# Performance work log

Measured on AMD Instinct MI355X. Metric: run time of the kernel, lower is better.

Reference implementation:

```python
import jax, jax.numpy as jnp
import numpy as np

DIM = 64
HID = 2 * DIM  # ffn_expansion_factor hard-coded to 2 in __init__


def _conv(x, w, b, pad, groups=1):
    # x: [N,C,H,W], w: [O, C//groups, kh, kw] (torch OIHW layout)
    y = jax.lax.conv_general_dilated(
        x, w, window_strides=(1, 1), padding=[(pad, pad), (pad, pad)],
        feature_group_count=groups,
        dimension_numbers=('NCHW', 'OIHW', 'NCHW'))
    return y + b[None, :, None, None]


def setup_inputs() -> dict:
    key = jax.random.key(0)
    ks = jax.random.split(key, 16)
    s = 0.05
    B, H, W = 4, 256, 256
    return {
        'x': jax.random.normal(ks[0], (B, DIM, H, W), jnp.float32),
        'pneffectiveness': jax.random.normal(ks[1], (B, 2, H, W), jnp.float32),
        # project_in: dim -> 2*hidden, 1x1
        'w_in': jax.random.normal(ks[2], (2 * HID, DIM, 1, 1), jnp.float32) * s,
        'b_in': jax.random.normal(ks[3], (2 * HID,), jnp.float32) * s,
        # project_in_pn: 2 -> hidden, 1x1
        'w_pn': jax.random.normal(ks[4], (HID, 2, 1, 1), jnp.float32) * s,
        'b_pn': jax.random.normal(ks[5], (HID,), jnp.float32) * s,
        # dwconvI: 3*hidden -> hidden, 3x3, groups=hidden (3 in-ch per group)
        'w_dw1': jax.random.normal(ks[6], (HID, 3, 3, 3), jnp.float32) * s,
        'b_dw1': jax.random.normal(ks[7], (HID,), jnp.float32) * s,
        # dwconvIII[0]: 3*hidden -> hidden, 3x3, groups=hidden
        'w_dw3a': jax.random.normal(ks[8], (HID, 3, 3, 3), jnp.float32) * s,
        'b_dw3a': jax.random.normal(ks[9], (HID,), jnp.float32) * s,
        # dwconvIII[1]: hidden -> hidden depthwise 3x3
        'w_dw3b': jax.random.normal(ks[10], (HID, 1, 3, 3), jnp.float32) * s,
        'b_dw3b': jax.random.normal(ks[11], (HID,), jnp.float32) * s,
        # project_out: hidden -> dim, 1x1, groups=2
        'w_out': jax.random.normal(ks[12], (DIM, HID // 2, 1, 1), jnp.float32) * s,
        'b_out': jax.random.normal(ks[13], (DIM,), jnp.float32) * s,
    }


def reference(x, pneffectiveness, w_in, b_in, w_pn, b_pn, w_dw1, b_dw1,
              w_dw3a, b_dw3a, w_dw3b, b_dw3b, w_out, b_out):
    xi = _conv(x, w_in, b_in, pad=0)                    # [B, 2*HID, H, W]
    pn = _conv(pneffectiveness, w_pn, b_pn, pad=0)      # [B, HID, H, W]
    xc = jnp.concatenate([pn, xi], axis=1)              # [B, 3*HID, H, W]
    d1 = _conv(xc, w_dw1, b_dw1, pad=1, groups=HID)     # [B, HID, H, W]
    d3 = _conv(xc, w_dw3a, b_dw3a, pad=1, groups=HID)
    d3 = _conv(d3, w_dw3b, b_dw3b, pad=1, groups=HID)   # [B, HID, H, W]
    x1_a, x1_b = jnp.split(d1, 2, axis=1)
    x2_a, x2_b = jnp.split(d3, 2, axis=1)
    x1 = jnp.concatenate([x1_a, x2_a], axis=1)          # [B, HID, H, W]
    x2 = jnp.concatenate([x1_b, x2_b], axis=1)
    g = jax.nn.gelu(x1, approximate=False) * x2         # exact GELU like F.gelu
    return _conv(g, w_out, b_out, pad=0, groups=2)      # [B, DIM, H, W]
```

## Files before the change

kernel.cpp:

```cpp
#include <hip/hip_runtime.h>
#include <hip/hip_bf16.h>


#define T 16
#define R20 20
#define R18 18
#define HW 65536
#define XC_BYTES ((size_t)4 * 16 * HW * 24 * 2)

typedef unsigned short u16;
typedef unsigned int u32;

typedef __attribute__((ext_vector_type(8))) short bf16x8;
typedef __attribute__((ext_vector_type(4))) float f32x4;
typedef __attribute__((ext_vector_type(2))) float f32x2;

__device__ __forceinline__ float bflo(u32 w) {
    union { u32 i; float f; } v; v.i = w << 16; return v.f;
}
__device__ __forceinline__ float bfhi(u32 w) {
    union { u32 i; float f; } v; v.i = w & 0xffff0000u; return v.f;
}
__device__ __forceinline__ float bf2f(u16 u) {
    union { u32 i; float f; } v; v.i = ((u32)u) << 16; return v.f;
}
__device__ __forceinline__ u16 f2bf(float f) {
    union { float f; u32 i; } v; v.f = f;
    u32 x = v.i;
    u32 r = (x + 0x7fffu + ((x >> 16) & 1u)) >> 16;
    return (u16)r;
}
__device__ __forceinline__ u32 f2bf2(float a, float b) {
    return (u32)f2bf(a) | ((u32)f2bf(b) << 16);
}
__device__ __forceinline__ float gelu_exact(float v) {
    return 0.5f * v * (1.0f + erff(v * 0.70710678118654752f));
}
__device__ __forceinline__ float erf_fast(float x) {
    float ax = fabsf(x);
    float t = __builtin_amdgcn_rcpf(fmaf(0.3275911f, ax, 1.0f));
    float p = fmaf(t, 1.061405429f, -1.453152027f);
    p = fmaf(t, p, 1.421413741f);
    p = fmaf(t, p, -0.284496736f);
    p = fmaf(t, p, 0.254829592f);
    p = p * t;
    float e = __expf(-ax * ax);
    float r = fmaf(-p, e, 1.0f);
    return copysignf(r, x);
}
__device__ __forceinline__ float gelu_fast(float v) {
    return 0.5f * v * (1.0f + erf_fast(v * 0.70710678118654752f));
}

__device__ __forceinline__ void pack_pair(float a, float b, u32& hi, u32& lo) {
    union { float f; u32 i; } ua, ub, ha, hb, la, lb;
    ua.f = a; ub.f = b;
    ha.i = ua.i & 0xffff0000u;
    hb.i = ub.i & 0xffff0000u;
    hi = (ha.i >> 16) | hb.i;
    la.f = a - ha.f;
    lb.f = b - hb.f;
    lo = (la.i >> 16) | (lb.i & 0xffff0000u);
}

__global__ __launch_bounds__(256, 2)
void k1_proj_mfma(const float* __restrict__ xin,
                  const float* __restrict__ pnin,
                  const float* __restrict__ w_in,
                  const float* __restrict__ b_in,
                  const float* __restrict__ w_pn,
                  const float* __restrict__ b_pn,
                  u16* __restrict__ xc)
{
    __shared__ float s_x[64][65];
    __shared__ float s_bin[256];

    const int tid  = threadIdx.x;
    const int b    = blockIdx.y;
    const int px0  = blockIdx.x * 64;
    const int lane = tid & 63;
    const int wid  = tid >> 6;
    const int lr   = lane & 15;
    const int lh   = lane >> 4;
    const int CB   = wid * 64;

    s_bin[tid] = b_in[tid];

    {
        const float* xb = xin + (size_t)b * 64 * HW + px0;
#pragma unroll
        for (int i = 0; i < 4; ++i) {
            int idx = tid + 256 * i;
            int row = idx >> 4, seg = (idx & 15) * 4;
            float4 v = *(const float4*)(xb + (size_t)row * HW + seg);
            s_x[row][seg + 0] = v.x; s_x[row][seg + 1] = v.y;
            s_x[row][seg + 2] = v.z; s_x[row][seg + 3] = v.w;
        }
    }

    bf16x8 whi[4][2], wlo[4][2];
#pragma unroll
    for (int ci = 0; ci < 4; ++ci)
#pragma unroll
        for (int ks = 0; ks < 2; ++ks) {
            const float* wp = w_in + (size_t)(CB + 16 * ci + lr) * 64
                            + 32 * ks + 8 * lh;
            float4 A0 = *(const float4*)wp;
            float4 A1 = *(const float4*)(wp + 4);
            union { u32 u[4]; bf16x8 v; } H, L;
            pack_pair(A0.x, A0.y, H.u[0], L.u[0]);
            pack_pair(A0.z, A0.w, H.u[1], L.u[1]);
            pack_pair(A1.x, A1.y, H.u[2], L.u[2]);
            pack_pair(A1.z, A1.w, H.u[3], L.u[3]);
            whi[ci][ks] = H.v; wlo[ci][ks] = L.v;
        }

    {
        const int wu = __builtin_amdgcn_readfirstlane(wid);
        const int px = lane;
        float p0 = pnin[(size_t)b * 2 * HW + px0 + px];
        float p1 = pnin[(size_t)b * 2 * HW + HW + px0 + px];
#pragma unroll
        for (int q = 0; q < 8; ++q) {
            int k = 32 * wu + 4 * q;
            int c = k / 12, l = k - 12 * c;
            float v0 = fmaf(w_pn[2*k+0], p0, fmaf(w_pn[2*k+1], p1, b_pn[k+0]));
            float v1 = fmaf(w_pn[2*k+2], p0, fmaf(w_pn[2*k+3], p1, b_pn[k+1]));
            float v2 = fmaf(w_pn[2*k+4], p0, fmaf(w_pn[2*k+5], p1, b_pn[k+2]));
            float v3 = fmaf(w_pn[2*k+6], p0, fmaf(w_pn[2*k+7], p1, b_pn[k+3]));
            uint2 val;
            val.x = f2bf2(v0, v1);
            val.y = f2bf2(v2, v3);
            *(uint2*)(xc + ((size_t)(b * 16 + c) * HW + px0 + px) * 24 + l) = val;
        }
    }
    __syncthreads();

    f32x4 acc[4][4];
#pragma unroll
    for (int ci = 0; ci < 4; ++ci)
#pragma unroll
        for (int pj = 0; pj < 4; ++pj)
            acc[ci][pj] = (f32x4){0.f, 0.f, 0.f, 0.f};

#pragma unroll
    for (int pj = 0; pj < 4; ++pj) {
        bf16x8 xh[2], xl[2];
#pragma unroll
        for (int ks = 0; ks < 2; ++ks) {
            const int rb = 32 * ks + 8 * lh;
            const int cb = 16 * pj + lr;
            float x0 = s_x[rb + 0][cb], x1 = s_x[rb + 1][cb];
            float x2 = s_x[rb + 2][cb], x3 = s_x[rb + 3][cb];
            float x4 = s_x[rb + 4][cb], x5 = s_x[rb + 5][cb];
            float x6 = s_x[rb + 6][cb], x7 = s_x[rb + 7][cb];
            union { u32 u[4]; bf16x8 v; } H, L;
            pack_pair(x0, x1, H.u[0], L.u[0]);
            pack_pair(x2, x3, H.u[1], L.u[1]);
            pack_pair(x4, x5, H.u[2], L.u[2]);
            pack_pair(x6, x7, H.u[3], L.u[3]);
            xh[ks] = H.v; xl[ks] = L.v;
        }
#pragma unroll
        for (int ci = 0; ci < 4; ++ci) {
#pragma unroll
            for (int ks = 0; ks < 2; ++ks) {
                acc[ci][pj] = __builtin_amdgcn_mfma_f32_16x16x32_bf16(
                    whi[ci][ks], xh[ks], acc[ci][pj], 0, 0, 0);
                acc[ci][pj] = __builtin_amdgcn_mfma_f32_16x16x32_bf16(
                    whi[ci][ks], xl[ks], acc[ci][pj], 0, 0, 0);
                acc[ci][pj] = __builtin_amdgcn_mfma_f32_16x16x32_bf16(
                    wlo[ci][ks], xh[ks], acc[ci][pj], 0, 0, 0);
            }
        }
    }

#pragma unroll
    for (int ci = 0; ci < 4; ++ci) {
        const int kk = CB + 16 * ci + 4 * lh;
        float b0 = s_bin[kk + 0], b1 = s_bin[kk + 1];
        float b2 = s_bin[kk + 2], b3 = s_bin[kk + 3];
        int c, l;
        int kg = kk + 128;
        if (kg < 192) { c = kg / 12; l = kg - 12 * c; }
        else { int t2 = kg - 192; int cq = t2 / 12; c = cq; l = 12 + (t2 - 12 * cq); }
        u16* rec = xc + ((size_t)(b * 16 + c) * HW + px0) * 24 + l;
#pragma unroll
        for (int pj = 0; pj < 4; ++pj) {
            f32x4 a = acc[ci][pj];
            uint2 val;
            val.x = f2bf2(a[0] + b0, a[1] + b1);
            val.y = f2bf2(a[2] + b2, a[3] + b3);
            *(uint2*)(rec + (size_t)(16 * pj + lr) * 24) = val;
        }
    }
}

__global__ __launch_bounds__(512, 2)
void k2_spatial(const u16* __restrict__ xc,
                const float* __restrict__ w_dw1,  const float* __restrict__ b_dw1,
                const float* __restrict__ w_dw3a, const float* __restrict__ b_dw3a,
                const float* __restrict__ w_dw3b, const float* __restrict__ b_dw3b,
                const float* __restrict__ w_out,  const float* __restrict__ b_out,
                float* __restrict__ outp)
{
    __shared__ __align__(8) u16 s_xc[24][R20 * R20];
    __shared__ __align__(8) u16 s_d3a[8][R18 * R18];
    __shared__ __align__(8) u16 s_d1[8][T * T];
    __shared__ __align__(8) u16 s_d3[8][T * T];
    __shared__ float s_woutT[64 * 66];
    __shared__ float s_wd1[8][27];
    __shared__ float s_wd3a[8][27];
    __shared__ float s_wd3b[8][9];
    __shared__ float s_b1[8], s_b3a[8], s_b3b[8];

    const int tid  = threadIdx.x;
    const int half = tid >> 8;
    const int pix  = tid & 255;
    const int ox0 = blockIdx.x * T;
    const int oy0 = blockIdx.y * T;
    const int b   = blockIdx.z;
    const int ob  = half * 32;

    for (int i = tid; i < 4096; i += 512) {
        int o = i >> 6, c = i & 63;
        s_woutT[c * 66 + o] = w_out[i];
    }

    int hpy = tid / R20, hpx = tid - hpy * R20;
    int hgy = oy0 - 2 + hpy, hgx = ox0 - 2 + hpx;
    const bool pvalid = (tid < 400) &&
                        ((unsigned)hgy < 256u) && ((unsigned)hgx < 256u);
    const u16* psrc = xc + ((size_t)(b * 16) * HW
                            + (pvalid ? (hgy * 256 + hgx) : 0)) * 24;
    uint4 pv0, pv1, pv2;
    pv0 = pv1 = pv2 = make_uint4(0, 0, 0, 0);
    if (pvalid) {
        const uint4* s = (const uint4*)psrc;
        pv0 = s[0]; pv1 = s[1]; pv2 = s[2];
    }

    f32x2 acc2[16];
#pragma unroll
    for (int o = 0; o < 16; ++o) acc2[o] = (f32x2){0.f, 0.f};

    for (int chunk = 0; chunk < 16; ++chunk) {
        const int c0 = chunk * 4;
        __syncthreads();

        {
            int t = tid;
            if (t < 216) {
                int gl = t / 27, idx = t - gl * 27;
                int g = (gl < 4) ? (c0 + gl) : (c0 + 60 + gl);
                s_wd1[gl][idx] = w_dw1[g * 27 + idx];
            } else if (t < 432) {
                int t2 = t - 216;
                int gl = t2 / 27, idx = t2 - gl * 27;
                int g = (gl < 4) ? (c0 + gl) : (c0 + 60 + gl);
                s_wd3a[gl][idx] = w_dw3a[g * 27 + idx];
            } else if (t < 504) {
                int t2 = t - 432;
                int gl = t2 / 9, idx = t2 - gl * 9;
                int g = (gl < 4) ? (c0 + gl) : (c0 + 60 + gl);
                s_wd3b[gl][idx] = w_dw3b[g * 9 + idx];
            } else if (t < 512) {
                int gl = t - 504;
                int g = (gl < 4) ? (c0 + gl) : (c0 + 60 + gl);
                s_b1[gl]  = b_dw1[g];
                s_b3a[gl] = b_dw3a[g];
                s_b3b[gl] = b_dw3b[g];
            }
        }

        if (tid < 400) {
            union { uint4 q[3]; u16 h[24]; } v;
            v.q[0] = pv0; v.q[1] = pv1; v.q[2] = pv2;
#pragma unroll
            for (int l = 0; l < 24; ++l) s_xc[l][tid] = v.h[l];
        }
        {
            uint4 n0, n1, n2;
            n0 = n1 = n2 = make_uint4(0, 0, 0, 0);
            if (pvalid && chunk < 15) {
                const uint4* s = (const uint4*)(psrc
                                 + (size_t)(chunk + 1) * HW * 24);
                n0 = s[0]; n1 = s[1]; n2 = s[2];
            }
            pv0 = n0; pv1 = n1; pv2 = n2;
        }
        __syncthreads();

        for (int task = tid; task < 8 * 81; task += 512) {
            int gl = task / 81, patch = task - gl * 81;
            int py = (patch / 9) * 2, px = (patch - (patch / 9) * 9) * 2;
            float bias = s_b3a[gl];
            float a00 = bias, a01 = bias, a10 = bias, a11 = bias;
#pragma unroll
            for (int j = 0; j < 3; ++j) {
                int lc = (gl < 4) ? (3 * gl + j) : (12 + 3 * (gl - 4) + j);
                const u32* base = (const u32*)&s_xc[lc][0];
                float win[4][4];
#pragma unroll
                for (int r = 0; r < 4; ++r) {
                    int e = (py + r) * R20 + px;
                    u32 u0 = base[e >> 1];
                    u32 u1 = base[(e >> 1) + 1];
                    win[r][0] = bflo(u0); win[r][1] = bfhi(u0);
                    win[r][2] = bflo(u1); win[r][3] = bfhi(u1);
                }
#pragma unroll
                for (int ky = 0; ky < 3; ++ky)
#pragma unroll
                    for (int kx = 0; kx < 3; ++kx) {
                        float wgt = s_wd3a[gl][j * 9 + ky * 3 + kx];
                        a00 = fmaf(wgt, win[ky][kx], a00);
                        a01 = fmaf(wgt, win[ky][kx + 1], a01);
                        a10 = fmaf(wgt, win[ky + 1][kx], a10);
                        a11 = fmaf(wgt, win[ky + 1][kx + 1], a11);
                    }
            }
            int gy0 = oy0 - 1 + py, gx0 = ox0 - 1 + px;
            bool vy0 = (unsigned)gy0 < 256u, vy1 = (unsigned)(gy0 + 1) < 256u;
            bool vx0 = (unsigned)gx0 < 256u, vx1 = (unsigned)(gx0 + 1) < 256u;
            u16* drow = &s_d3a[gl][py * R18 + px];
            drow[0]       = (vy0 && vx0) ? f2bf(a00) : (u16)0;
            drow[1]       = (vy0 && vx1) ? f2bf(a01) : (u16)0;
            drow[R18]     = (vy1 && vx0) ? f2bf(a10) : (u16)0;
            drow[R18 + 1] = (vy1 && vx1) ? f2bf(a11) : (u16)0;
        }

        {
            int gl = tid >> 6, patch = tid & 63;
            int py = (patch >> 3) * 2, px = (patch & 7) * 2;
            float bias = s_b1[gl];
            float a00 = bias, a01 = bias, a10 = bias, a11 = bias;
#pragma unroll
            for (int j = 0; j < 3; ++j) {
                int lc = (gl < 4) ? (3 * gl + j) : (12 + 3 * (gl - 4) + j);
                const u32* base = (const u32*)&s_xc[lc][0];
                float win[4][4];
#pragma unroll
                for (int r = 0; r < 4; ++r) {
                    int e = (py + 1 + r) * R20 + px;
                    u32 u0 = base[e >> 1];
                    u32 u1 = base[(e >> 1) + 1];
                    u32 u2 = base[(e >> 1) + 2];
                    win[r][0] = bfhi(u0); win[r][1] = bflo(u1);
                    win[r][2] = bfhi(u1); win[r][3] = bflo(u2);
                }
#pragma unroll
                for (int ky = 0; ky < 3; ++ky)
#pragma unroll
                    for (int kx = 0; kx < 3; ++kx) {
                        float wgt = s_wd1[gl][j * 9 + ky * 3 + kx];
                        a00 = fmaf(wgt, win[ky][kx], a00);
                        a01 = fmaf(wgt, win[ky][kx + 1], a01);
                        a10 = fmaf(wgt, win[ky + 1][kx], a10);
                        a11 = fmaf(wgt, win[ky + 1][kx + 1], a11);
                    }
            }
            u16* drow = &s_d1[gl][py * T + px];
            drow[0] = f2bf(a00); drow[1] = f2bf(a01);
            drow[T] = f2bf(a10); drow[T + 1] = f2bf(a11);
        }
        __syncthreads();

        {
            int gl = tid >> 6, patch = tid & 63;
            int py = (patch >> 3) * 2, px = (patch & 7) * 2;
            float bias = s_b3b[gl];
            float a00 = bias, a01 = bias, a10 = bias, a11 = bias;
            float win[4][4];
            const u32* base = (const u32*)&s_d3a[gl][0];
#pragma unroll
            for (int r = 0; r < 4; ++r) {
                int e = (py + r) * R18 + px;
                u32 u0 = base[e >> 1];
                u32 u1 = base[(e >> 1) + 1];
                win[r][0] = bflo(u0); win[r][1] = bfhi(u0);
                win[r][2] = bflo(u1); win[r][3] = bfhi(u1);
            }
#pragma unroll
            for (int ky = 0; ky < 3; ++ky)
#pragma unroll
                for (int kx = 0; kx < 3; ++kx) {
                    float wgt = s_wd3b[gl][ky * 3 + kx];
                    a00 = fmaf(wgt, win[ky][kx], a00);
                    a01 = fmaf(wgt, win[ky][kx + 1], a01);
                    a10 = fmaf(wgt, win[ky + 1][kx], a10);
                    a11 = fmaf(wgt, win[ky + 1][kx + 1], a11);
                }
            u16* drow = &s_d3[gl][py * T + px];
            drow[0] = f2bf(a00); drow[1] = f2bf(a01);
            drow[T] = f2bf(a10); drow[T + 1] = f2bf(a11);
        }
        __syncthreads();

        {
            const u16* sD = (half == 0) ? &s_d1[0][0] : &s_d3[0][0];
#pragma unroll
            for (int jp = 0; jp < 2; ++jp) {
                int j0 = 2 * jp;
                float ga = gelu_fast(bf2f(sD[j0 * 256 + pix]))
                         * bf2f(sD[(j0 + 4) * 256 + pix]);
                float gb = gelu_fast(bf2f(sD[(j0 + 1) * 256 + pix]))
                         * bf2f(sD[(j0 + 5) * 256 + pix]);
                int c = c0 + j0;
                const float* wc0 = &s_woutT[(c + 0) * 66 + ob];
                const float* wc1 = &s_woutT[(c + 1) * 66 + ob];
                f32x2 ga2 = {ga, ga}, gb2 = {gb, gb};
#pragma unroll
                for (int o = 0; o < 16; ++o) {
                    f32x2 w0 = *(const f32x2*)(wc0 + 2 * o);
                    f32x2 w1 = *(const f32x2*)(wc1 + 2 * o);
                    acc2[o] = __builtin_elementwise_fma(w0, ga2, acc2[o]);
                    acc2[o] = __builtin_elementwise_fma(w1, gb2, acc2[o]);
                }
            }
        }
    }

    {
        int py = pix >> 4, pxx = pix & 15;
        size_t obase = (size_t)b * 64 * HW + (size_t)ob * HW
                     + (size_t)(oy0 + py) * 256 + (ox0 + pxx);
#pragma unroll
        for (int o = 0; o < 16; ++o) {
            outp[obase + (size_t)(2 * o + 0) * HW] = acc2[o][0] + b_out[ob + 2 * o + 0];
            outp[obase + (size_t)(2 * o + 1) * HW] = acc2[o][1] + b_out[ob + 2 * o + 1];
        }
    }
}

__global__ __launch_bounds__(256, 2)
void ffd_fused(const float* __restrict__ xin, const float* __restrict__ pnin,
               const float* __restrict__ w_in, const float* __restrict__ b_in,
               const float* __restrict__ w_pn, const float* __restrict__ b_pn,
               const float* __restrict__ w_dw1, const float* __restrict__ b_dw1,
               const float* __restrict__ w_dw3a, const float* __restrict__ b_dw3a,
               const float* __restrict__ w_dw3b, const float* __restrict__ b_dw3b,
               const float* __restrict__ w_out, const float* __restrict__ b_out,
               float* __restrict__ outp)
{
    __shared__ __align__(8) u16 s_xc[24][R20 * R20];
    __shared__ __align__(8) float s_d3a[8][R18 * R18];
    __shared__ float s_d1[8][T * T];
    __shared__ float s_d3[8][T * T];
    __shared__ float s_wd1[8][27];
    __shared__ float s_wd3a[8][27];
    __shared__ float s_wd3b[8][9];
    __shared__ float s_b1[8], s_b3a[8], s_b3b[8];

    const int tid = threadIdx.x;
    const int ox0 = blockIdx.x * T;
    const int oy0 = blockIdx.y * T;
    const int b   = blockIdx.z;

    float accL[32], accH[32];
#pragma unroll
    for (int o = 0; o < 32; ++o) { accL[o] = 0.f; accH[o] = 0.f; }

    for (int chunk = 0; chunk < 16; ++chunk) {
        const int c0 = chunk * 4;
        __syncthreads();

        for (int t = tid; t < 512; t += 256) {
            if (t < 216) {
                int gl = t / 27, idx = t - gl * 27;
                int g = (gl < 4) ? (c0 + gl) : (c0 + 60 + gl);
                s_wd1[gl][idx] = w_dw1[g * 27 + idx];
            } else if (t < 432) {
                int t2 = t - 216;
                int gl = t2 / 27, idx = t2 - gl * 27;
                int g = (gl < 4) ? (c0 + gl) : (c0 + 60 + gl);
                s_wd3a[gl][idx] = w_dw3a[g * 27 + idx];
            } else if (t < 504) {
                int t2 = t - 432;
                int gl = t2 / 9, idx = t2 - gl * 9;
                int g = (gl < 4) ? (c0 + gl) : (c0 + 60 + gl);
                s_wd3b[gl][idx] = w_dw3b[g * 9 + idx];
            } else {
                int gl = t - 504;
                int g = (gl < 4) ? (c0 + gl) : (c0 + 60 + gl);
                s_b1[gl]  = b_dw1[g];
                s_b3a[gl] = b_dw3a[g];
                s_b3b[gl] = b_dw3b[g];
            }
        }

        for (int p = tid; p < R20 * R20; p += 256) {
            int py = p / R20, px = p - py * R20;
            int gy = oy0 - 2 + py, gx = ox0 - 2 + px;
            if ((unsigned)gy >= 256u || (unsigned)gx >= 256u) {
#pragma unroll 1
                for (int l = 0; l < 24; ++l) s_xc[l][p] = 0;
                continue;
            }
            const int off = gy * 256 + gx;
            float xr[64];
            const float* xp = xin + (size_t)b * 64 * HW + off;
#pragma unroll
            for (int c = 0; c < 64; ++c) xr[c] = xp[(size_t)c * HW];
            float p0 = 0.f, p1 = 0.f;
            if (3 * c0 < 128) {
                const float* pp = pnin + (size_t)b * 2 * HW + off;
                p0 = pp[0]; p1 = pp[HW];
            }
#pragma unroll 1
            for (int l = 0; l < 24; ++l) {
                int k = (l < 12) ? (3 * c0 + l) : (3 * c0 + 192 + (l - 12));
                float acc;
                if (k < 128) {
// ... 91 lines not shown
        for (int task = tid; task < 8 * 64; task += 256) {
            int gl = task >> 6, patch = task & 63;
            int py = (patch >> 3) * 2, px = (patch & 7) * 2;
            float bias = s_b3b[gl];
            float a00 = bias, a01 = bias, a10 = bias, a11 = bias;
            float win[4][4];
#pragma unroll
            for (int r = 0; r < 4; ++r) {
                int e = (py + r) * R18 + px;
                float2 f0 = *(const float2*)&s_d3a[gl][e];
                float2 f1 = *(const float2*)&s_d3a[gl][e + 2];
                win[r][0] = f0.x; win[r][1] = f0.y;
                win[r][2] = f1.x; win[r][3] = f1.y;
            }
#pragma unroll
            for (int ky = 0; ky < 3; ++ky)
#pragma unroll
                for (int kx = 0; kx < 3; ++kx) {
                    float wgt = s_wd3b[gl][ky * 3 + kx];
                    a00 = fmaf(wgt, win[ky][kx], a00);
                    a01 = fmaf(wgt, win[ky][kx + 1], a01);
                    a10 = fmaf(wgt, win[ky + 1][kx], a10);
                    a11 = fmaf(wgt, win[ky + 1][kx + 1], a11);
                }
            float* drow = &s_d3[gl][py * T + px];
            drow[0] = a00; drow[1] = a01; drow[T] = a10; drow[T + 1] = a11;
        }
        __syncthreads();

#pragma unroll
        for (int jp = 0; jp < 2; ++jp) {
            int j0 = 2 * jp;
            float g1a = gelu_exact(s_d1[j0][tid])     * s_d1[j0 + 4][tid];
            float g1b = gelu_exact(s_d1[j0 + 1][tid]) * s_d1[j0 + 5][tid];
            float g2a = gelu_exact(s_d3[j0][tid])     * s_d3[j0 + 4][tid];
            float g2b = gelu_exact(s_d3[j0 + 1][tid]) * s_d3[j0 + 5][tid];
            int c = c0 + j0;
#pragma unroll
            for (int o = 0; o < 32; ++o) {
                float2 wL = *(const float2*)(w_out + o * 64 + c);
                accL[o] = fmaf(wL.x, g1a, accL[o]);
                accL[o] = fmaf(wL.y, g1b, accL[o]);
                float2 wH = *(const float2*)(w_out + (o + 32) * 64 + c);
                accH[o] = fmaf(wH.x, g2a, accH[o]);
                accH[o] = fmaf(wH.y, g2b, accH[o]);
            }
        }
    }

    {
        int py = tid >> 4, pxx = tid & 15;
        size_t obase = (size_t)b * 64 * HW
                     + (size_t)(oy0 + py) * 256 + (ox0 + pxx);
#pragma unroll
        for (int o = 0; o < 32; ++o) {
            outp[obase + (size_t)o * HW]        = accL[o] + b_out[o];
            outp[obase + (size_t)(o + 32) * HW] = accH[o] + b_out[o + 32];
        }
    }
}

extern "C" void kernel_launch(void* const* d_in, const int* in_sizes, int n_in,
                              void* d_out, int out_size, void* d_ws, size_t ws_size,
                              hipStream_t stream) {
    (void)in_sizes; (void)n_in; (void)out_size;
    const float* xin    = (const float*)d_in[0];
    const float* pnin   = (const float*)d_in[1];
    const float* w_in   = (const float*)d_in[2];
    const float* b_in   = (const float*)d_in[3];
    const float* w_pn   = (const float*)d_in[4];
    const float* b_pn   = (const float*)d_in[5];
    const float* w_dw1  = (const float*)d_in[6];
    const float* b_dw1  = (const float*)d_in[7];
    const float* w_dw3a = (const float*)d_in[8];
    const float* b_dw3a = (const float*)d_in[9];
    const float* w_dw3b = (const float*)d_in[10];
    const float* b_dw3b = (const float*)d_in[11];
    const float* w_out  = (const float*)d_in[12];
    const float* b_out  = (const float*)d_in[13];
    float* outp = (float*)d_out;

    if (ws_size >= XC_BYTES) {
        u16* xc = (u16*)d_ws;
        dim3 g1(1024, 4), b1(256);
        k1_proj_mfma<<<g1, b1, 0, stream>>>(xin, pnin, w_in, b_in, w_pn, b_pn, xc);
        dim3 g2(16, 16, 4), b2(512);
        k2_spatial<<<g2, b2, 0, stream>>>(xc, w_dw1, b_dw1, w_dw3a, b_dw3a,
                                          w_dw3b, b_dw3b, w_out, b_out, outp);
    } else {
        dim3 grid(16, 16, 4), blk(256);
        ffd_fused<<<grid, blk, 0, stream>>>(xin, pnin, w_in, b_in, w_pn, b_pn,
                                            w_dw1, b_dw1, w_dw3a, b_dw3a,
                                            w_dw3b, b_dw3b, w_out, b_out, outp);
    }
}
```

Measured before the change: 507.2 us.

## Persist k1 blocks over four tiles with prefetch; fuse k2 dw1/dw3b into GELU stage

k1 now processes four 64-pixel tiles per block. It keeps its converted weights in registers and prefetches the next x tile into a double-buffered shared array while the MFMAs run, so the grid shrinks to a quarter of its former size. k2 stores the halo tiles and the intermediate dw3a results as fp32 in shared memory. Each thread pair computes dw1 and dw3b per pixel directly, exchanges the GELU products with a lane shuffle and feeds project_out, which removes the bf16 d1/d3 staging buffers and one barrier. The cost is more shared memory in k2, which may lower occupancy, and more redundant neighbourhood reads per thread.

```diff
diff --git a/kernel.cpp b/kernel.cpp
--- a/kernel.cpp
+++ b/kernel.cpp
@@ -72,31 +72,20 @@
                   const float* __restrict__ b_pn,
                   u16* __restrict__ xc)
 {
-    __shared__ float s_x[64][65];
+    __shared__ float s_x[2][64][65];
     __shared__ float s_bin[256];
 
     const int tid  = threadIdx.x;
     const int b    = blockIdx.y;
-    const int px0  = blockIdx.x * 64;
+    const int pxbase = blockIdx.x * 256;
     const int lane = tid & 63;
     const int wid  = tid >> 6;
     const int lr   = lane & 15;
     const int lh   = lane >> 4;
     const int CB   = wid * 64;
+    const int wu   = __builtin_amdgcn_readfirstlane(wid);
 
     s_bin[tid] = b_in[tid];
-
-    {
-        const float* xb = xin + (size_t)b * 64 * HW + px0;
-#pragma unroll
-        for (int i = 0; i < 4; ++i) {
-            int idx = tid + 256 * i;
-            int row = idx >> 4, seg = (idx & 15) * 4;
-            float4 v = *(const float4*)(xb + (size_t)row * HW + seg);
-            s_x[row][seg + 0] = v.x; s_x[row][seg + 1] = v.y;
-            s_x[row][seg + 2] = v.z; s_x[row][seg + 3] = v.w;
-        }
-    }
 
     bf16x8 whi[4][2], wlo[4][2];
 #pragma unroll
@@ -116,10 +105,37 @@
         }
 
     {
-        const int wu = __builtin_amdgcn_readfirstlane(wid);
-        const int px = lane;
-        float p0 = pnin[(size_t)b * 2 * HW + px0 + px];
-        float p1 = pnin[(size_t)b * 2 * HW + HW + px0 + px];
+        const float* xb = xin + (size_t)b * 64 * HW + pxbase;
+#pragma unroll
+        for (int i = 0; i < 4; ++i) {
+            int idx = tid + 256 * i;
+            int row = idx >> 4, seg = (idx & 15) * 4;
+            float4 v = *(const float4*)(xb + (size_t)row * HW + seg);
+            s_x[0][row][seg + 0] = v.x; s_x[0][row][seg + 1] = v.y;
+            s_x[0][row][seg + 2] = v.z; s_x[0][row][seg + 3] = v.w;
+        }
+    }
+
+    int cur = 0;
+#pragma unroll 1
+    for (int t = 0; t < 4; ++t) {
+        const int px0 = pxbase + t * 64;
+
+        float4 nx[4];
+        if (t < 3) {
+            const float* xb = xin + (size_t)b * 64 * HW + px0 + 64;
+#pragma unroll
+            for (int i = 0; i < 4; ++i) {
+                int idx = tid + 256 * i;
+                int row = idx >> 4, seg = (idx & 15) * 4;
+                nx[i] = *(const float4*)(xb + (size_t)row * HW + seg);
+            }
+        }
+        float p0 = pnin[(size_t)b * 2 * HW + px0 + lane];
+        float p1 = pnin[(size_t)b * 2 * HW + HW + px0 + lane];
+
+        __syncthreads();
+
 #pragma unroll
         for (int q = 0; q < 8; ++q) {
             int k = 32 * wu + 4 * q;
@@ -131,67 +147,77 @@
             uint2 val;
             val.x = f2bf2(v0, v1);
             val.y = f2bf2(v2, v3);
-            *(uint2*)(xc + ((size_t)(b * 16 + c) * HW + px0 + px) * 24 + l) = val;
-        }
-    }
-    __syncthreads();
-
-    f32x4 acc[4][4];
-#pragma unroll
-    for (int ci = 0; ci < 4; ++ci)
-#pragma unroll
-        for (int pj = 0; pj < 4; ++pj)
-            acc[ci][pj] = (f32x4){0.f, 0.f, 0.f, 0.f};
-
-#pragma unroll
-    for (int pj = 0; pj < 4; ++pj) {
-        bf16x8 xh[2], xl[2];
-#pragma unroll
-        for (int ks = 0; ks < 2; ++ks) {
-            const int rb = 32 * ks + 8 * lh;
-            const int cb = 16 * pj + lr;
-            float x0 = s_x[rb + 0][cb], x1 = s_x[rb + 1][cb];
-            float x2 = s_x[rb + 2][cb], x3 = s_x[rb + 3][cb];
-            float x4 = s_x[rb + 4][cb], x5 = s_x[rb + 5][cb];
-            float x6 = s_x[rb + 6][cb], x7 = s_x[rb + 7][cb];
-            union { u32 u[4]; bf16x8 v; } H, L;
-            pack_pair(x0, x1, H.u[0], L.u[0]);
-            pack_pair(x2, x3, H.u[1], L.u[1]);
-            pack_pair(x4, x5, H.u[2], L.u[2]);
-            pack_pair(x6, x7, H.u[3], L.u[3]);
-            xh[ks] = H.v; xl[ks] = L.v;
-        }
+            *(uint2*)(xc + ((size_t)(b * 16 + c) * HW + px0 + lane) * 24 + l) = val;
+        }
+
+        f32x4 acc[4][4];
+#pragma unroll
+        for (int ci = 0; ci < 4; ++ci)
+#pragma unroll
+            for (int pj = 0; pj < 4; ++pj)
+                acc[ci][pj] = (f32x4){0.f, 0.f, 0.f, 0.f};
+
+#pragma unroll
+        for (int pj = 0; pj < 4; ++pj) {
+            bf16x8 xh[2], xl[2];
+#pragma unroll
+            for (int ks = 0; ks < 2; ++ks) {
+                const int rb = 32 * ks + 8 * lh;
+                const int cb = 16 * pj + lr;
+                float x0 = s_x[cur][rb + 0][cb], x1 = s_x[cur][rb + 1][cb];
+                float x2 = s_x[cur][rb + 2][cb], x3 = s_x[cur][rb + 3][cb];
+                float x4 = s_x[cur][rb + 4][cb], x5 = s_x[cur][rb + 5][cb];
+                float x6 = s_x[cur][rb + 6][cb], x7 = s_x[cur][rb + 7][cb];
+                union { u32 u[4]; bf16x8 v; } H, L;
+                pack_pair(x0, x1, H.u[0], L.u[0]);
+                pack_pair(x2, x3, H.u[1], L.u[1]);
+                pack_pair(x4, x5, H.u[2], L.u[2]);
+                pack_pair(x6, x7, H.u[3], L.u[3]);
+                xh[ks] = H.v; xl[ks] = L.v;
+            }
+#pragma unroll
+            for (int ci = 0; ci < 4; ++ci) {
+#pragma unroll
+                for (int ks = 0; ks < 2; ++ks) {
+                    acc[ci][pj] = __builtin_amdgcn_mfma_f32_16x16x32_bf16(
+                        whi[ci][ks], xh[ks], acc[ci][pj], 0, 0, 0);
+                    acc[ci][pj] = __builtin_amdgcn_mfma_f32_16x16x32_bf16(
+                        whi[ci][ks], xl[ks], acc[ci][pj], 0, 0, 0);
+                    acc[ci][pj] = __builtin_amdgcn_mfma_f32_16x16x32_bf16(
+                        wlo[ci][ks], xh[ks], acc[ci][pj], 0, 0, 0);
+                }
+            }
+        }
+
 #pragma unroll
         for (int ci = 0; ci < 4; ++ci) {
-#pragma unroll
-            for (int ks = 0; ks < 2; ++ks) {
-                acc[ci][pj] = __builtin_amdgcn_mfma_f32_16x16x32_bf16(
-                    whi[ci][ks], xh[ks], acc[ci][pj], 0, 0, 0);
-                acc[ci][pj] = __builtin_amdgcn_mfma_f32_16x16x32_bf16(
-                    whi[ci][ks], xl[ks], acc[ci][pj], 0, 0, 0);
-                acc[ci][pj] = __builtin_amdgcn_mfma_f32_16x16x32_bf16(
-                    wlo[ci][ks], xh[ks], acc[ci][pj], 0, 0, 0);
-            }
-        }
-    }
-
-#pragma unroll
-    for (int ci = 0; ci < 4; ++ci) {
-        const int kk = CB + 16 * ci + 4 * lh;
-        float b0 = s_bin[kk + 0], b1 = s_bin[kk + 1];
-        float b2 = s_bin[kk + 2], b3 = s_bin[kk + 3];
-        int c, l;
-        int kg = kk + 128;
-        if (kg < 192) { c = kg / 12; l = kg - 12 * c; }
-        else { int t2 = kg - 192; int cq = t2 / 12; c = cq; l = 12 + (t2 - 12 * cq); }
-        u16* rec = xc + ((size_t)(b * 16 + c) * HW + px0) * 24 + l;
-#pragma unroll
-        for (int pj = 0; pj < 4; ++pj) {
-            f32x4 a = acc[ci][pj];
-            uint2 val;
-            val.x = f2bf2(a[0] + b0, a[1] + b1);
-            val.y = f2bf2(a[2] + b2, a[3] + b3);
-            *(uint2*)(rec + (size_t)(16 * pj + lr) * 24) = val;
+            const int kk = CB + 16 * ci + 4 * lh;
+            float b0 = s_bin[kk + 0], b1 = s_bin[kk + 1];
+            float b2 = s_bin[kk + 2], b3 = s_bin[kk + 3];
+            int c, l;
+            int kg = kk + 128;
+            if (kg < 192) { c = kg / 12; l = kg - 12 * c; }
+            else { int t2 = kg - 192; int cq = t2 / 12; c = cq; l = 12 + (t2 - 12 * cq); }
+            u16* rec = xc + ((size_t)(b * 16 + c) * HW + px0) * 24 + l;
+#pragma unroll
+            for (int pj = 0; pj < 4; ++pj) {
+                f32x4 a = acc[ci][pj];
+                uint2 val;
+                val.x = f2bf2(a[0] + b0, a[1] + b1);
+                val.y = f2bf2(a[2] + b2, a[3] + b3);
+                *(uint2*)(rec + (size_t)(16 * pj + lr) * 24) = val;
+            }
+        }
+
+        if (t < 3) {
+#pragma unroll
+            for (int i = 0; i < 4; ++i) {
+                int idx = tid + 256 * i;
+                int row = idx >> 4, seg = (idx & 15) * 4;
+                float* d = &s_x[cur ^ 1][row][seg];
+                d[0] = nx[i].x; d[1] = nx[i].y; d[2] = nx[i].z; d[3] = nx[i].w;
+            }
+            cur ^= 1;
         }
     }
 }
@@ -204,23 +230,21 @@
                 const float* __restrict__ w_out,  const float* __restrict__ b_out,
                 float* __restrict__ outp)
 {
-    __shared__ __align__(8) u16 s_xc[24][R20 * R20];
-    __shared__ __align__(8) u16 s_d3a[8][R18 * R18];
-    __shared__ __align__(8) u16 s_d1[8][T * T];
-    __shared__ __align__(8) u16 s_d3[8][T * T];
+    __shared__ float s_xc32[24][R20 * R20];
+    __shared__ float s_d3a32[8][R18 * R18];
     __shared__ float s_woutT[64 * 66];
     __shared__ float s_wd1[8][27];
     __shared__ float s_wd3a[8][27];
     __shared__ float s_wd3b[8][9];
     __shared__ float s_b1[8], s_b3a[8], s_b3b[8];
 
-    const int tid  = threadIdx.x;
-    const int half = tid >> 8;
-    const int pix  = tid & 255;
+    const int tid = threadIdx.x;
+    const int pix = tid >> 1;
+    const int sub = tid & 1;
+    const int ob  = sub * 32;
     const int ox0 = blockIdx.x * T;
     const int oy0 = blockIdx.y * T;
     const int b   = blockIdx.z;
-    const int ob  = half * 32;
 
     for (int i = tid; i < 4096; i += 512) {
         int o = i >> 6, c = i & 63;
@@ -277,7 +301,7 @@
             union { uint4 q[3]; u16 h[24]; } v;
             v.q[0] = pv0; v.q[1] = pv1; v.q[2] = pv2;
 #pragma unroll
-            for (int l = 0; l < 24; ++l) s_xc[l][tid] = v.h[l];
+            for (int l = 0; l < 24; ++l) s_xc32[l][tid] = bf2f(v.h[l]);
         }
         {
             uint4 n0, n1, n2;
@@ -299,15 +323,14 @@
 #pragma unroll
             for (int j = 0; j < 3; ++j) {
                 int lc = (gl < 4) ? (3 * gl + j) : (12 + 3 * (gl - 4) + j);
-                const u32* base = (const u32*)&s_xc[lc][0];
+                const float* base = &s_xc32[lc][py * R20 + px];
                 float win[4][4];
 #pragma unroll
                 for (int r = 0; r < 4; ++r) {
-                    int e = (py + r) * R20 + px;
-                    u32 u0 = base[e >> 1];
-                    u32 u1 = base[(e >> 1) + 1];
-                    win[r][0] = bflo(u0); win[r][1] = bfhi(u0);
-                    win[r][2] = bflo(u1); win[r][3] = bfhi(u1);
+                    float2 f0 = *(const float2*)(base + r * R20);
+                    float2 f1 = *(const float2*)(base + r * R20 + 2);
+                    win[r][0] = f0.x; win[r][1] = f0.y;
+                    win[r][2] = f1.x; win[r][3] = f1.y;
                 }
 #pragma unroll
                 for (int ky = 0; ky < 3; ++ky)
@@ -323,99 +346,64 @@
             int gy0 = oy0 - 1 + py, gx0 = ox0 - 1 + px;
             bool vy0 = (unsigned)gy0 < 256u, vy1 = (unsigned)(gy0 + 1) < 256u;
             bool vx0 = (unsigned)gx0 < 256u, vx1 = (unsigned)(gx0 + 1) < 256u;
-            u16* drow = &s_d3a[gl][py * R18 + px];
-            drow[0]       = (vy0 && vx0) ? f2bf(a00) : (u16)0;
-            drow[1]       = (vy0 && vx1) ? f2bf(a01) : (u16)0;
-            drow[R18]     = (vy1 && vx0) ? f2bf(a10) : (u16)0;
-            drow[R18 + 1] = (vy1 && vx1) ? f2bf(a11) : (u16)0;
-        }
+            float* drow = &s_d3a32[gl][py * R18 + px];
+            drow[0]       = (vy0 && vx0) ? a00 : 0.f;
+            drow[1]       = (vy0 && vx1) ? a01 : 0.f;
+            drow[R18]     = (vy1 && vx0) ? a10 : 0.f;
+            drow[R18 + 1] = (vy1 && vx1) ? a11 : 0.f;
+        }
+        __syncthreads();
 
         {
-            int gl = tid >> 6, patch = tid & 63;
-            int py = (patch >> 3) * 2, px = (patch & 7) * 2;
-            float bias = s_b1[gl];
-            float a00 = bias, a01 = bias, a10 = bias, a11 = bias;
-#pragma unroll
-            for (int j = 0; j < 3; ++j) {
-                int lc = (gl < 4) ? (3 * gl + j) : (12 + 3 * (gl - 4) + j);
-                const u32* base = (const u32*)&s_xc[lc][0];
-                float win[4][4];
-#pragma unroll
-                for (int r = 0; r < 4; ++r) {
-                    int e = (py + 1 + r) * R20 + px;
-                    u32 u0 = base[e >> 1];
-                    u32 u1 = base[(e >> 1) + 1];
-                    u32 u2 = base[(e >> 1) + 2];
-                    win[r][0] = bfhi(u0); win[r][1] = bflo(u1);
-                    win[r][2] = bfhi(u1); win[r][3] = bflo(u2);
-                }
-#pragma unroll
-                for (int ky = 0; ky < 3; ++ky)
-#pragma unroll
-                    for (int kx = 0; kx < 3; ++kx) {
-                        float wgt = s_wd1[gl][j * 9 + ky * 3 + kx];
-                        a00 = fmaf(wgt, win[ky][kx], a00);
-                        a01 = fmaf(wgt, win[ky][kx + 1], a01);
-                        a10 = fmaf(wgt, win[ky + 1][kx], a10);
-                        a11 = fmaf(wgt, win[ky + 1][kx + 1], a11);
+            const int py = pix >> 4, px = pix & 15;
+            float d1v[4], d3v[4];
+#pragma unroll
+            for (int i = 0; i < 4; ++i) {
+                const int gl = 2 * sub + (i & 1) + 4 * (i >> 1);
+                float a = s_b1[gl];
+#pragma unroll
+                for (int j = 0; j < 3; ++j) {
+                    int lc = (gl < 4) ? (3 * gl + j) : (12 + 3 * (gl - 4) + j);
+                    const float* w9 = &s_wd1[gl][j * 9];
+                    const float* xr = &s_xc32[lc][(py + 1) * R20 + px + 1];
+#pragma unroll
+                    for (int ky = 0; ky < 3; ++ky) {
+                        a = fmaf(w9[ky * 3 + 0], xr[ky * R20 + 0], a);
+                        a = fmaf(w9[ky * 3 + 1], xr[ky * R20 + 1], a);
+                        a = fmaf(w9[ky * 3 + 2], xr[ky * R20 + 2], a);
                     }
-            }
-            u16* drow = &s_d1[gl][py * T + px];
-            drow[0] = f2bf(a00); drow[1] = f2bf(a01);
-            drow[T] = f2bf(a10); drow[T + 1] = f2bf(a11);
-        }
-        __syncthreads();
-
-        {
-            int gl = tid >> 6, patch = tid & 63;
-            int py = (patch >> 3) * 2, px = (patch & 7) * 2;
-            float bias = s_b3b[gl];
-            float a00 = bias, a01 = bias, a10 = bias, a11 = bias;
-            float win[4][4];
-            const u32* base = (const u32*)&s_d3a[gl][0];
-#pragma unroll
-            for (int r = 0; r < 4; ++r) {
-                int e = (py + r) * R18 + px;
-                u32 u0 = base[e >> 1];
-                u32 u1 = base[(e >> 1) + 1];
-                win[r][0] = bflo(u0); win[r][1] = bfhi(u0);
-                win[r][2] = bflo(u1); win[r][3] = bfhi(u1);
-            }
-#pragma unroll
-            for (int ky = 0; ky < 3; ++ky)
-#pragma unroll
-                for (int kx = 0; kx < 3; ++kx) {
-                    float wgt = s_wd3b[gl][ky * 3 + kx];
-                    a00 = fmaf(wgt, win[ky][kx], a00);
-                    a01 = fmaf(wgt, win[ky][kx + 1], a01);
-                    a10 = fmaf(wgt, win[ky + 1][kx], a10);
-                    a11 = fmaf(wgt, win[ky + 1][kx + 1], a11);
-                }
-            u16* drow = &s_d3[gl][py * T + px];
-            drow[0] = f2bf(a00); drow[1] = f2bf(a01);
-            drow[T] = f2bf(a10); drow[T + 1] = f2bf(a11);
-        }
-        __syncthreads();
-
-        {
-            const u16* sD = (half == 0) ? &s_d1[0][0] : &s_d3[0][0];
-#pragma unroll
-            for (int jp = 0; jp < 2; ++jp) {
-                int j0 = 2 * jp;
-                float ga = gelu_fast(bf2f(sD[j0 * 256 + pix]))
-                         * bf2f(sD[(j0 + 4) * 256 + pix]);
-                float gb = gelu_fast(bf2f(sD[(j0 + 1) * 256 + pix]))
-                         * bf2f(sD[(j0 + 5) * 256 + pix]);
-                int c = c0 + j0;
-                const float* wc0 = &s_woutT[(c + 0) * 66 + ob];
-                const float* wc1 = &s_woutT[(c + 1) * 66 + ob];
-                f32x2 ga2 = {ga, ga}, gb2 = {gb, gb};
+                }
+                d1v[i] = a;
+                float dv = s_b3b[gl];
+                const float* w9b = &s_wd3b[gl][0];
+                const float* dr = &s_d3a32[gl][py * R18 + px];
+#pragma unroll
+                for (int ky = 0; ky < 3; ++ky) {
+                    dv = fmaf(w9b[ky * 3 + 0], dr[ky * R18 + 0], dv);
+                    dv = fmaf(w9b[ky * 3 + 1], dr[ky * R18 + 1], dv);
+                    dv = fmaf(w9b[ky * 3 + 2], dr[ky * R18 + 2], dv);
+                }
+                d3v[i] = dv;
+            }
+            float p1a = gelu_fast(d1v[0]) * d1v[2];
+            float p1b = gelu_fast(d1v[1]) * d1v[3];
+            float p3a = gelu_fast(d3v[0]) * d3v[2];
+            float p3b = gelu_fast(d3v[1]) * d3v[3];
+            float r0 = __shfl_xor(sub ? p1a : p3a, 1);
+            float r1 = __shfl_xor(sub ? p1b : p3b, 1);
+            float g0 = sub ? r0 : p1a;
+            float g1 = sub ? r1 : p1b;
+            float g2 = sub ? p3a : r0;
+            float g3 = sub ? p3b : r1;
+            const float gprod[4] = {g0, g1, g2, g3};
+#pragma unroll
+            for (int j = 0; j < 4; ++j) {
+                const float* wc = &s_woutT[(c0 + j) * 66 + ob];
+                f32x2 gj2 = {gprod[j], gprod[j]};
 #pragma unroll
                 for (int o = 0; o < 16; ++o) {
-                    f32x2 w0 = *(const f32x2*)(wc0 + 2 * o);
-                    f32x2 w1 = *(const f32x2*)(wc1 + 2 * o);
-                    acc2[o] = __builtin_elementwise_fma(w0, ga2, acc2[o]);
-                    acc2[o] = __builtin_elementwise_fma(w1, gb2, acc2[o]);
+                    f32x2 w2 = *(const f32x2*)(wc + 2 * o);
+                    acc2[o] = __builtin_elementwise_fma(w2, gj2, acc2[o]);
                 }
             }
         }
@@ -686,7 +674,7 @@
 
     if (ws_size >= XC_BYTES) {
         u16* xc = (u16*)d_ws;
-        dim3 g1(1024, 4), b1(256);
+        dim3 g1(256, 4), b1(256);
         k1_proj_mfma<<<g1, b1, 0, stream>>>(xin, pnin, w_in, b_in, w_pn, b_pn, xc);
         dim3 g2(16, 16, 4), b2(512);
         k2_spatial<<<g2, b2, 0, stream>>>(xc, w_dw1, b_dw1, w_dw3a, b_dw3a,
```

After: 698.2 us. 1.38x slower.

## Move project_out to bf16 MFMA and double-buffer x tiles in projection kernel

Applied to the files above, without the earlier changes.

In the spatial kernel, the grouped 1x1 output projection no longer runs as per-pixel scalar FMAs against a transposed weight table in shared memory. Gated GELU values are now staged as bf16 in shared memory and multiplied with split hi/lo bf16 weights using MFMA after every 32 channels. The projection kernel now processes four 64-pixel tiles per block and prefetches the next x tile into registers while the current one is computed, with a double-buffered shared tile. Rounding the activations to bf16 for the final matmul lowers precision. The larger blocks also cut the projection grid from 1024 to 256 blocks per batch, which reduces parallelism.

```diff
diff --git a/kernel.cpp b/kernel.cpp
--- a/kernel.cpp
+++ b/kernel.cpp
@@ -72,31 +72,20 @@
                   const float* __restrict__ b_pn,
                   u16* __restrict__ xc)
 {
-    __shared__ float s_x[64][65];
+    __shared__ float s_x[2][64][65];
     __shared__ float s_bin[256];
 
     const int tid  = threadIdx.x;
     const int b    = blockIdx.y;
-    const int px0  = blockIdx.x * 64;
+    const int pxbase = blockIdx.x * 256;
     const int lane = tid & 63;
     const int wid  = tid >> 6;
     const int lr   = lane & 15;
     const int lh   = lane >> 4;
     const int CB   = wid * 64;
+    const int wu   = __builtin_amdgcn_readfirstlane(wid);
 
     s_bin[tid] = b_in[tid];
-
-    {
-        const float* xb = xin + (size_t)b * 64 * HW + px0;
-#pragma unroll
-        for (int i = 0; i < 4; ++i) {
-            int idx = tid + 256 * i;
-            int row = idx >> 4, seg = (idx & 15) * 4;
-            float4 v = *(const float4*)(xb + (size_t)row * HW + seg);
-            s_x[row][seg + 0] = v.x; s_x[row][seg + 1] = v.y;
-            s_x[row][seg + 2] = v.z; s_x[row][seg + 3] = v.w;
-        }
-    }
 
     bf16x8 whi[4][2], wlo[4][2];
 #pragma unroll
@@ -116,10 +105,37 @@
         }
 
     {
-        const int wu = __builtin_amdgcn_readfirstlane(wid);
-        const int px = lane;
-        float p0 = pnin[(size_t)b * 2 * HW + px0 + px];
-        float p1 = pnin[(size_t)b * 2 * HW + HW + px0 + px];
+        const float* xb = xin + (size_t)b * 64 * HW + pxbase;
+#pragma unroll
+        for (int i = 0; i < 4; ++i) {
+            int idx = tid + 256 * i;
+            int row = idx >> 4, seg = (idx & 15) * 4;
+            float4 v = *(const float4*)(xb + (size_t)row * HW + seg);
+            s_x[0][row][seg + 0] = v.x; s_x[0][row][seg + 1] = v.y;
+            s_x[0][row][seg + 2] = v.z; s_x[0][row][seg + 3] = v.w;
+        }
+    }
+
+    int cur = 0;
+#pragma unroll 1
+    for (int t = 0; t < 4; ++t) {
+        const int px0 = pxbase + t * 64;
+
+        float4 nx[4];
+        if (t < 3) {
+            const float* xb = xin + (size_t)b * 64 * HW + px0 + 64;
+#pragma unroll
+            for (int i = 0; i < 4; ++i) {
+                int idx = tid + 256 * i;
+                int row = idx >> 4, seg = (idx & 15) * 4;
+                nx[i] = *(const float4*)(xb + (size_t)row * HW + seg);
+            }
+        }
+        float p0 = pnin[(size_t)b * 2 * HW + px0 + lane];
+        float p1 = pnin[(size_t)b * 2 * HW + HW + px0 + lane];
+
+        __syncthreads();
+
 #pragma unroll
         for (int q = 0; q < 8; ++q) {
             int k = 32 * wu + 4 * q;
@@ -131,67 +147,77 @@
             uint2 val;
             val.x = f2bf2(v0, v1);
             val.y = f2bf2(v2, v3);
-            *(uint2*)(xc + ((size_t)(b * 16 + c) * HW + px0 + px) * 24 + l) = val;
-        }
-    }
-    __syncthreads();
-
-    f32x4 acc[4][4];
-#pragma unroll
-    for (int ci = 0; ci < 4; ++ci)
-#pragma unroll
-        for (int pj = 0; pj < 4; ++pj)
-            acc[ci][pj] = (f32x4){0.f, 0.f, 0.f, 0.f};
-
-#pragma unroll
-    for (int pj = 0; pj < 4; ++pj) {
-        bf16x8 xh[2], xl[2];
-#pragma unroll
-        for (int ks = 0; ks < 2; ++ks) {
-            const int rb = 32 * ks + 8 * lh;
-            const int cb = 16 * pj + lr;
-            float x0 = s_x[rb + 0][cb], x1 = s_x[rb + 1][cb];
-            float x2 = s_x[rb + 2][cb], x3 = s_x[rb + 3][cb];
-            float x4 = s_x[rb + 4][cb], x5 = s_x[rb + 5][cb];
-            float x6 = s_x[rb + 6][cb], x7 = s_x[rb + 7][cb];
-            union { u32 u[4]; bf16x8 v; } H, L;
-            pack_pair(x0, x1, H.u[0], L.u[0]);
-            pack_pair(x2, x3, H.u[1], L.u[1]);
-            pack_pair(x4, x5, H.u[2], L.u[2]);
-            pack_pair(x6, x7, H.u[3], L.u[3]);
-            xh[ks] = H.v; xl[ks] = L.v;
-        }
+            *(uint2*)(xc + ((size_t)(b * 16 + c) * HW + px0 + lane) * 24 + l) = val;
+        }
+
+        f32x4 acc[4][4];
+#pragma unroll
+        for (int ci = 0; ci < 4; ++ci)
+#pragma unroll
+            for (int pj = 0; pj < 4; ++pj)
+                acc[ci][pj] = (f32x4){0.f, 0.f, 0.f, 0.f};
+
+#pragma unroll
+        for (int pj = 0; pj < 4; ++pj) {
+            bf16x8 xh[2], xl[2];
+#pragma unroll
+            for (int ks = 0; ks < 2; ++ks) {
+                const int rb = 32 * ks + 8 * lh;
+                const int cb = 16 * pj + lr;
+                float x0 = s_x[cur][rb + 0][cb], x1 = s_x[cur][rb + 1][cb];
+                float x2 = s_x[cur][rb + 2][cb], x3 = s_x[cur][rb + 3][cb];
+                float x4 = s_x[cur][rb + 4][cb], x5 = s_x[cur][rb + 5][cb];
+                float x6 = s_x[cur][rb + 6][cb], x7 = s_x[cur][rb + 7][cb];
+                union { u32 u[4]; bf16x8 v; } H, L;
+                pack_pair(x0, x1, H.u[0], L.u[0]);
+                pack_pair(x2, x3, H.u[1], L.u[1]);
+                pack_pair(x4, x5, H.u[2], L.u[2]);
+                pack_pair(x6, x7, H.u[3], L.u[3]);
+                xh[ks] = H.v; xl[ks] = L.v;
+            }
+#pragma unroll
+            for (int ci = 0; ci < 4; ++ci) {
+#pragma unroll
+                for (int ks = 0; ks < 2; ++ks) {
+                    acc[ci][pj] = __builtin_amdgcn_mfma_f32_16x16x32_bf16(
+                        whi[ci][ks], xh[ks], acc[ci][pj], 0, 0, 0);
+                    acc[ci][pj] = __builtin_amdgcn_mfma_f32_16x16x32_bf16(
+                        whi[ci][ks], xl[ks], acc[ci][pj], 0, 0, 0);
+                    acc[ci][pj] = __builtin_amdgcn_mfma_f32_16x16x32_bf16(
+                        wlo[ci][ks], xh[ks], acc[ci][pj], 0, 0, 0);
+                }
+            }
+        }
+
 #pragma unroll
         for (int ci = 0; ci < 4; ++ci) {
-#pragma unroll
-            for (int ks = 0; ks < 2; ++ks) {
-                acc[ci][pj] = __builtin_amdgcn_mfma_f32_16x16x32_bf16(
-                    whi[ci][ks], xh[ks], acc[ci][pj], 0, 0, 0);
-                acc[ci][pj] = __builtin_amdgcn_mfma_f32_16x16x32_bf16(
-                    whi[ci][ks], xl[ks], acc[ci][pj], 0, 0, 0);
-                acc[ci][pj] = __builtin_amdgcn_mfma_f32_16x16x32_bf16(
-                    wlo[ci][ks], xh[ks], acc[ci][pj], 0, 0, 0);
-            }
-        }
-    }
-
-#pragma unroll
-    for (int ci = 0; ci < 4; ++ci) {
-        const int kk = CB + 16 * ci + 4 * lh;
-        float b0 = s_bin[kk + 0], b1 = s_bin[kk + 1];
-        float b2 = s_bin[kk + 2], b3 = s_bin[kk + 3];
-        int c, l;
-        int kg = kk + 128;
-        if (kg < 192) { c = kg / 12; l = kg - 12 * c; }
-        else { int t2 = kg - 192; int cq = t2 / 12; c = cq; l = 12 + (t2 - 12 * cq); }
-        u16* rec = xc + ((size_t)(b * 16 + c) * HW + px0) * 24 + l;
-#pragma unroll
-        for (int pj = 0; pj < 4; ++pj) {
-            f32x4 a = acc[ci][pj];
-            uint2 val;
-            val.x = f2bf2(a[0] + b0, a[1] + b1);
-            val.y = f2bf2(a[2] + b2, a[3] + b3);
-            *(uint2*)(rec + (size_t)(16 * pj + lr) * 24) = val;
+            const int kk = CB + 16 * ci + 4 * lh;
+            float b0 = s_bin[kk + 0], b1 = s_bin[kk + 1];
+            float b2 = s_bin[kk + 2], b3 = s_bin[kk + 3];
+            int c, l;
+            int kg = kk + 128;
+            if (kg < 192) { c = kg / 12; l = kg - 12 * c; }
+            else { int t2 = kg - 192; int cq = t2 / 12; c = cq; l = 12 + (t2 - 12 * cq); }
+            u16* rec = xc + ((size_t)(b * 16 + c) * HW + px0) * 24 + l;
+#pragma unroll
+            for (int pj = 0; pj < 4; ++pj) {
+                f32x4 a = acc[ci][pj];
+                uint2 val;
+                val.x = f2bf2(a[0] + b0, a[1] + b1);
+                val.y = f2bf2(a[2] + b2, a[3] + b3);
+                *(uint2*)(rec + (size_t)(16 * pj + lr) * 24) = val;
+            }
+        }
+
+        if (t < 3) {
+#pragma unroll
+            for (int i = 0; i < 4; ++i) {
+                int idx = tid + 256 * i;
+                int row = idx >> 4, seg = (idx & 15) * 4;
+                float* d = &s_x[cur ^ 1][row][seg];
+                d[0] = nx[i].x; d[1] = nx[i].y; d[2] = nx[i].z; d[3] = nx[i].w;
+            }
+            cur ^= 1;
         }
     }
 }
@@ -208,7 +234,7 @@
     __shared__ __align__(8) u16 s_d3a[8][R18 * R18];
     __shared__ __align__(8) u16 s_d1[8][T * T];
     __shared__ __align__(8) u16 s_d3[8][T * T];
-    __shared__ float s_woutT[64 * 66];
+    __shared__ __align__(16) u16 s_g[2][256][40];
     __shared__ float s_wd1[8][27];
     __shared__ float s_wd3a[8][27];
     __shared__ float s_wd3b[8][9];
@@ -220,12 +246,14 @@
     const int ox0 = blockIdx.x * T;
     const int oy0 = blockIdx.y * T;
     const int b   = blockIdx.z;
-    const int ob  = half * 32;
-
-    for (int i = tid; i < 4096; i += 512) {
-        int o = i >> 6, c = i & 63;
-        s_woutT[c * 66 + o] = w_out[i];
-    }
+
+    const int w    = tid >> 6;
+    const int lane = tid & 63;
+    const int lr   = lane & 15;
+    const int lh   = lane >> 4;
+    const int gh   = w >> 2;
+    const int cw   = (w >> 1) & 1;
+    const int ph   = w & 1;
 
     int hpy = tid / R20, hpx = tid - hpy * R20;
     int hgy = oy0 - 2 + hpy, hgx = ox0 - 2 + hpx;
@@ -240,9 +268,9 @@
         pv0 = s[0]; pv1 = s[1]; pv2 = s[2];
     }
 
-    f32x2 acc2[16];
-#pragma unroll
-    for (int o = 0; o < 16; ++o) acc2[o] = (f32x2){0.f, 0.f};
+    f32x4 acc[8];
+#pragma unroll
+    for (int t = 0; t < 8; ++t) acc[t] = (f32x4){0.f, 0.f, 0.f, 0.f};
 
     for (int chunk = 0; chunk < 16; ++chunk) {
         const int c0 = chunk * 4;
@@ -399,36 +427,52 @@
 
         {
             const u16* sD = (half == 0) ? &s_d1[0][0] : &s_d3[0][0];
-#pragma unroll
-            for (int jp = 0; jp < 2; ++jp) {
-                int j0 = 2 * jp;
-                float ga = gelu_fast(bf2f(sD[j0 * 256 + pix]))
-                         * bf2f(sD[(j0 + 4) * 256 + pix]);
-                float gb = gelu_fast(bf2f(sD[(j0 + 1) * 256 + pix]))
-                         * bf2f(sD[(j0 + 5) * 256 + pix]);
-                int c = c0 + j0;
-                const float* wc0 = &s_woutT[(c + 0) * 66 + ob];
-                const float* wc1 = &s_woutT[(c + 1) * 66 + ob];
-                f32x2 ga2 = {ga, ga}, gb2 = {gb, gb};
-#pragma unroll
-                for (int o = 0; o < 16; ++o) {
-                    f32x2 w0 = *(const f32x2*)(wc0 + 2 * o);
-                    f32x2 w1 = *(const f32x2*)(wc1 + 2 * o);
-                    acc2[o] = __builtin_elementwise_fma(w0, ga2, acc2[o]);
-                    acc2[o] = __builtin_elementwise_fma(w1, gb2, acc2[o]);
-                }
+            float ga = gelu_fast(bf2f(sD[0 * 256 + pix])) * bf2f(sD[4 * 256 + pix]);
+            float gb = gelu_fast(bf2f(sD[1 * 256 + pix])) * bf2f(sD[5 * 256 + pix]);
+            float gc = gelu_fast(bf2f(sD[2 * 256 + pix])) * bf2f(sD[6 * 256 + pix]);
+            float gd = gelu_fast(bf2f(sD[3 * 256 + pix])) * bf2f(sD[7 * 256 + pix]);
+            uint2 val;
+            val.x = f2bf2(ga, gb);
+            val.y = f2bf2(gc, gd);
+            *(uint2*)&s_g[half][pix][c0 & 31] = val;
+        }
+
+        if (chunk == 7 || chunk == 15) {
+            __syncthreads();
+            const int p = chunk >> 3;
+            const float* wp = w_out + (size_t)(32 * gh + 16 * cw + lr) * 64
+                            + 32 * p + 8 * lh;
+            float4 A0 = *(const float4*)wp;
+            float4 A1 = *(const float4*)(wp + 4);
+            union { u32 u[4]; bf16x8 v; } H, L;
+            pack_pair(A0.x, A0.y, H.u[0], L.u[0]);
+            pack_pair(A0.z, A0.w, H.u[1], L.u[1]);
+            pack_pair(A1.x, A1.y, H.u[2], L.u[2]);
+            pack_pair(A1.z, A1.w, H.u[3], L.u[3]);
+            bf16x8 Ah = H.v, Al = L.v;
+#pragma unroll
+            for (int t = 0; t < 8; ++t) {
+                int pt = 8 * ph + t;
+                bf16x8 Bv = *(const bf16x8*)&s_g[gh][16 * pt + lr][8 * lh];
+                acc[t] = __builtin_amdgcn_mfma_f32_16x16x32_bf16(Ah, Bv, acc[t], 0, 0, 0);
+                acc[t] = __builtin_amdgcn_mfma_f32_16x16x32_bf16(Al, Bv, acc[t], 0, 0, 0);
             }
         }
     }
 
     {
-        int py = pix >> 4, pxx = pix & 15;
-        size_t obase = (size_t)b * 64 * HW + (size_t)ob * HW
-                     + (size_t)(oy0 + py) * 256 + (ox0 + pxx);
-#pragma unroll
-        for (int o = 0; o < 16; ++o) {
-            outp[obase + (size_t)(2 * o + 0) * HW] = acc2[o][0] + b_out[ob + 2 * o + 0];
-            outp[obase + (size_t)(2 * o + 1) * HW] = acc2[o][1] + b_out[ob + 2 * o + 1];
+        const int o = 32 * gh + 16 * cw + 4 * lh;
+        float b0 = b_out[o + 0], b1 = b_out[o + 1];
+        float b2 = b_out[o + 2], b3 = b_out[o + 3];
+#pragma unroll
+        for (int t = 0; t < 8; ++t) {
+            int pt = 8 * ph + t;
+            size_t base = (size_t)b * 64 * HW + (size_t)o * HW
+                        + (size_t)(oy0 + pt) * 256 + (ox0 + lr);
+            outp[base + 0 * HW] = acc[t][0] + b0;
+            outp[base + 1 * HW] = acc[t][1] + b1;
+            outp[base + 2 * HW] = acc[t][2] + b2;
+            outp[base + 3 * HW] = acc[t][3] + b3;
         }
     }
 }
@@ -686,7 +730,7 @@
 
     if (ws_size >= XC_BYTES) {
         u16* xc = (u16*)d_ws;
-        dim3 g1(1024, 4), b1(256);
+        dim3 g1(256, 4), b1(256);
         k1_proj_mfma<<<g1, b1, 0, stream>>>(xin, pnin, w_in, b_in, w_pn, b_pn, xc);
         dim3 g2(16, 16, 4), b2(512);
         k2_spatial<<<g2, b2, 0, stream>>>(xc, w_dw1, b_dw1, w_dw3a, b_dw3a,
```

New measurement: 463.6 us, median of 2. 8.6% less time.
